# Kernel tuning notes

Hardware: AMD Instinct MI355X
Metric: run time of the kernel (lower is better)

## Reference

```python
import jax, jax.numpy as jnp
import numpy as np

TEMPERATURE = 12.5      # args_temperature
SINKHORN_EPS = 0.05     # entropic regularization replacing exact cv2.EMD
SINKHORN_ITERS = 100


def _sinkhorn_flow(cost, a, b):
    # cost: [N, hw, hw] (rows=query nodes, cols=proto nodes)
    # a: [N, hw] row marginals, b: [N, hw] col marginals (each sums to hw)
    K = jnp.exp(-cost / SINKHORN_EPS)
    v0 = jnp.ones_like(b)

    def body(v, _):
        u = a / (jnp.einsum('nuv,nv->nu', K, v) + 1e-30)
        v = b / (jnp.einsum('nuv,nu->nv', K, u) + 1e-30)
        return v, None

    v, _ = jax.lax.scan(body, v0, None, length=SINKHORN_ITERS)
    u = a / (jnp.einsum('nuv,nv->nu', K, v) + 1e-30)
    return u[:, :, None] * K * v[:, None, :]  # transport plan [N, hw, hw]


def setup_inputs() -> dict:
    key = jax.random.key(0)
    k1, k2 = jax.random.split(key)
    shape = (8, 5, 15, 640, 5, 5)  # (b, n2, n1, c, h, w)
    return {
        'in_support': jax.random.normal(k1, shape, jnp.float32),
        'in_query': jax.random.normal(k2, shape, jnp.float32),
    }


def reference(in_support, in_query):
    b, n2, n1, c, h, w = in_support.shape
    N, hw = b * n2 * n1, h * w
    S = in_support.reshape(N, c, hw)  # support/proto nodes
    Q = in_query.reshape(N, c, hw)    # query nodes

    # get_weight_vector: relu(<node, global-avg-pool(other)>) + 0.001
    w1 = jax.nn.relu(jnp.einsum('nck,nc->nk', Q, S.mean(-1))) + 0.001  # query-side
    w2 = jax.nn.relu(jnp.einsum('nck,nc->nk', S, Q.mean(-1))) + 0.001  # proto-side

    # normalize_feature: subtract per-sample channel mean ('center')
    S = S - S.mean(axis=1, keepdims=True)
    Q = Q - Q.mean(axis=1, keepdims=True)

    # cosine similarity map: sim[u, v] = cos(query_node_u, proto_node_v)
    Sn = S / jnp.maximum(jnp.linalg.norm(S, axis=1, keepdims=True), 1e-8)
    Qn = Q / jnp.maximum(jnp.linalg.norm(Q, axis=1, keepdims=True), 1e-8)
    sim = jnp.einsum('ncu,ncv->nuv', Qn, Sn)  # [N, hw, hw]

    # emd marginals: (w + 1e-5) rescaled so each sums to hw
    a = w1 + 1e-5
    a = a * (hw / a.sum(-1, keepdims=True))
    bm = w2 + 1e-5
    bm = bm * (hw / bm.sum(-1, keepdims=True))

    # OT flow on cost = 1 - sim (flow treated as a constant, like cv2 detach)
    flow = jax.lax.stop_gradient(_sinkhorn_flow(1.0 - sim, a, bm))

    return (sim * flow).sum((-1, -2)) * (TEMPERATURE / hw)  # logits [N]
```

## Files before the change

### kernel.cpp

```cpp
#include <hip/hip_runtime.h>

typedef short bf16x8 __attribute__((ext_vector_type(8)));
typedef float f32x4  __attribute__((ext_vector_type(4)));

constexpr int C  = 640;
constexpr int HW = 25;

__device__ __forceinline__ float rl(float x, int lane) {
  return __uint_as_float(__builtin_amdgcn_readlane(__float_as_uint(x), lane));
}

__device__ __forceinline__ void packpair(float x0, float x1, unsigned& h, unsigned& l) {
  unsigned u0 = __float_as_uint(x0), u1 = __float_as_uint(x1);
  h = __builtin_amdgcn_perm(u1, u0, 0x07060302u);
  float l0 = x0 - __uint_as_float(u0 & 0xFFFF0000u);
  float l1 = x1 - __uint_as_float(u1 & 0xFFFF0000u);
  l = __builtin_amdgcn_perm(__float_as_uint(l1), __float_as_uint(l0), 0x07060302u);
}

__global__ __launch_bounds__(256) void emd_fused(
    const float* __restrict__ support, const float* __restrict__ query,
    float* __restrict__ out)
{
  const int n = blockIdx.x, tid = threadIdx.x;
  const int wid = tid >> 6, lane = tid & 63;
  const int lg = lane >> 4, lr = lane & 15;

  __shared__ float accbuf[4][64][16];
  __shared__ float mombuf[4][8][64];
  __shared__ float G[625];
  __shared__ float sQv[25], sSv[25], nqv[25], nsv[25], amv[25], bmv[25], scal[2];

  const float* Qg = query   + (size_t)n * C * HW;
  const float* Sg = support + (size_t)n * C * HW;

  f32x4 acc[2][2];
  {
    f32x4 z = {0.f, 0.f, 0.f, 0.f};
    acc[0][0] = z; acc[0][1] = z; acc[1][0] = z; acc[1][1] = z;
  }
  float mq[2] = {0.f, 0.f}, mq2[2] = {0.f, 0.f};
  float ms[2] = {0.f, 0.f}, ms2[2] = {0.f, 0.f};

  #pragma unroll 1
  for (int s = 0; s < 5; ++s) {
    const int c0 = wid * 160 + s * 32 + lg * 8;
    const float* qb = Qg + c0 * HW;
    const float* sb = Sg + c0 * HW;
    bf16x8 Ah[2], Al[2], Bh[2], Bl[2];
    #pragma unroll
    for (int t = 0; t < 2; ++t) {
      const int row = t * 16 + lr;
      const bool ok = row < 25;
      float xq[8], xs[8];
      #pragma unroll
      for (int j = 0; j < 8; ++j) {
        xq[j] = ok ? qb[j * HW + row] : 0.f;
        xs[j] = ok ? sb[j * HW + row] : 0.f;
      }
      #pragma unroll
      for (int j = 0; j < 8; ++j) {
        mq[t] += xq[j]; mq2[t] = fmaf(xq[j], xq[j], mq2[t]);
        ms[t] += xs[j]; ms2[t] = fmaf(xs[j], xs[j], ms2[t]);
      }
      union { unsigned u[4]; bf16x8 v; } ah, al, bh, bl;
      #pragma unroll
      for (int jj = 0; jj < 4; ++jj) {
        packpair(xq[2 * jj], xq[2 * jj + 1], ah.u[jj], al.u[jj]);
        packpair(xs[2 * jj], xs[2 * jj + 1], bh.u[jj], bl.u[jj]);
      }
      Ah[t] = ah.v; Al[t] = al.v; Bh[t] = bh.v; Bl[t] = bl.v;
    }
    #pragma unroll
    for (int tr = 0; tr < 2; ++tr)
      #pragma unroll
      for (int tc = 0; tc < 2; ++tc) {
        acc[tr][tc] = __builtin_amdgcn_mfma_f32_16x16x32_bf16(Ah[tr], Bh[tc], acc[tr][tc], 0, 0, 0);
        acc[tr][tc] = __builtin_amdgcn_mfma_f32_16x16x32_bf16(Ah[tr], Bl[tc], acc[tr][tc], 0, 0, 0);
        acc[tr][tc] = __builtin_amdgcn_mfma_f32_16x16x32_bf16(Al[tr], Bh[tc], acc[tr][tc], 0, 0, 0);
      }
  }

  #pragma unroll
  for (int tr = 0; tr < 2; ++tr)
    #pragma unroll
    for (int tc = 0; tc < 2; ++tc)
      *reinterpret_cast<f32x4*>(&accbuf[wid][lane][(tr * 2 + tc) * 4]) = acc[tr][tc];
  mombuf[wid][0][lane] = mq[0];  mombuf[wid][1][lane] = mq[1];
  mombuf[wid][2][lane] = mq2[0]; mombuf[wid][3][lane] = mq2[1];
  mombuf[wid][4][lane] = ms[0];  mombuf[wid][5][lane] = ms[1];
  mombuf[wid][6][lane] = ms2[0]; mombuf[wid][7][lane] = ms2[1];
  __syncthreads();

  if (tid < 64) {
    #pragma unroll
    for (int q = 0; q < 4; ++q) {
      f32x4 rsum = *reinterpret_cast<const f32x4*>(&accbuf[0][lane][q * 4]);
      #pragma unroll
      for (int w = 1; w < 4; ++w)
        rsum += *reinterpret_cast<const f32x4*>(&accbuf[w][lane][q * 4]);
      const int tr = q >> 1, tc = q & 1;
      #pragma unroll
      for (int i = 0; i < 4; ++i) {
        int u = tr * 16 + (lane >> 4) * 4 + i;
        int v = tc * 16 + (lane & 15);
        if (u < 25 && v < 25) G[u * 25 + v] = rsum[i];
      }
    }
  }
  __syncthreads();

  if (tid < 25) {
    const int t = (tid < 16) ? 0 : 1, rr = tid - t * 16;
    float s = 0.f, ss = 0.f;
    #pragma unroll
    for (int w = 0; w < 4; ++w)
      #pragma unroll
      for (int gg = 0; gg < 4; ++gg) {
        s  += mombuf[w][0 + t][gg * 16 + rr];
        ss += mombuf[w][2 + t][gg * 16 + rr];
      }
    sQv[tid] = s;
    float var = ss - s * s * (1.f / C);
    nqv[tid] = fmaxf(sqrtf(fmaxf(var, 0.f)), 1e-8f);
    float rs = 0.f;
    #pragma unroll
    for (int j = 0; j < 25; ++j) rs += G[tid * 25 + j];
    amv[tid] = fmaxf(rs * (1.f / 25.f), 0.f) + 0.001f + 1e-5f;
  } else if (tid >= 32 && tid < 57) {
    const int v = tid - 32;
    const int t = (v < 16) ? 0 : 1, rr = v - t * 16;
    float s = 0.f, ss = 0.f;
    #pragma unroll
    for (int w = 0; w < 4; ++w)
      #pragma unroll
      for (int gg = 0; gg < 4; ++gg) {
        s  += mombuf[w][4 + t][gg * 16 + rr];
        ss += mombuf[w][6 + t][gg * 16 + rr];
      }
    sSv[v] = s;
    float var = ss - s * s * (1.f / C);
    nsv[v] = fmaxf(sqrtf(fmaxf(var, 0.f)), 1e-8f);
    float cs = 0.f;
    #pragma unroll
    for (int u = 0; u < 25; ++u) cs += G[u * 25 + v];
    bmv[v] = fmaxf(cs * (1.f / 25.f), 0.f) + 0.001f + 1e-5f;
  }
  __syncthreads();
  if (tid == 0)  { float s = 0.f; for (int i = 0; i < 25; ++i) s += amv[i]; scal[0] = 25.f / s; }
  if (tid == 64) { float s = 0.f; for (int i = 0; i < 25; ++i) s += bmv[i]; scal[1] = 25.f / s; }
  __syncthreads();
  for (int p = tid; p < 625; p += 256) {
    int u = p / 25, v = p % 25;
    float cov = G[p] - sQv[u] * sSv[v] * (1.f / C);
    G[p] = cov / (nqv[u] * nsv[v]);
  }
  __syncthreads();

  if (tid >= 64) return;
  const int u = (tid < 25) ? tid : 24;
  float simr[25], Krow[25], Kcol[25];
  #pragma unroll
  for (int j = 0; j < 25; ++j) simr[j] = G[u * 25 + j];
  #pragma unroll
  for (int j = 0; j < 25; ++j) Kcol[j] = __expf(-20.f * (1.f - G[j * 25 + u]));
  #pragma unroll
  for (int j = 0; j < 25; ++j) Krow[j] = __expf(-20.f * (1.f - simr[j]));
  const float a_u = amv[u] * scal[0], b_u = bmv[u] * scal[1];

  float vv = 1.0f, uu = 0.0f, vold = 1.0f;
  #pragma unroll 1
  for (int it = 0; it < 100; ++it) {
    float s0 = 0, s1 = 0, s2 = 0, s3 = 0, s4 = 0;
    #pragma unroll
    for (int j = 0; j < 25; j += 5) {
      s0 = fmaf(Krow[j + 0], rl(vv, j + 0), s0);
      s1 = fmaf(Krow[j + 1], rl(vv, j + 1), s1);
      s2 = fmaf(Krow[j + 2], rl(vv, j + 2), s2);
      s3 = fmaf(Krow[j + 3], rl(vv, j + 3), s3);
      s4 = fmaf(Krow[j + 4], rl(vv, j + 4), s4);
    }
    uu = a_u * __builtin_amdgcn_rcpf(((((s0 + s1) + (s2 + s3)) + s4) + 1e-30f));

    s0 = s1 = s2 = s3 = s4 = 0;
    #pragma unroll
    for (int j = 0; j < 25; j += 5) {
      s0 = fmaf(Kcol[j + 0], rl(uu, j + 0), s0);
      s1 = fmaf(Kcol[j + 1], rl(uu, j + 1), s1);
      s2 = fmaf(Kcol[j + 2], rl(uu, j + 2), s2);
      s3 = fmaf(Kcol[j + 3], rl(uu, j + 3), s3);
      s4 = fmaf(Kcol[j + 4], rl(uu, j + 4), s4);
    }
    vv = b_u * __builtin_amdgcn_rcpf(((((s0 + s1) + (s2 + s3)) + s4) + 1e-30f));

    if ((it & 1) == 1) {
      bool conv = fabsf(vv - vold) <= 1e-4f * fabsf(vv);
      if (__all(conv)) break;
      vold = vv;
    }
  }
  {
    float s0 = 0, s1 = 0, s2 = 0, s3 = 0, s4 = 0;
    #pragma unroll
    for (int j = 0; j < 25; j += 5) {
      s0 = fmaf(Krow[j + 0], rl(vv, j + 0), s0);
      s1 = fmaf(Krow[j + 1], rl(vv, j + 1), s1);
      s2 = fmaf(Krow[j + 2], rl(vv, j + 2), s2);
      s3 = fmaf(Krow[j + 3], rl(vv, j + 3), s3);
      s4 = fmaf(Krow[j + 4], rl(vv, j + 4), s4);
    }
    uu = a_u * __builtin_amdgcn_rcpf(((((s0 + s1) + (s2 + s3)) + s4) + 1e-30f));
  }

  float pr = 0.f;
  if (tid < 25) {
    float t0 = 0.f;
    #pragma unroll
    for (int j = 0; j < 25; ++j)
      t0 = fmaf(simr[j] * Krow[j], rl(vv, j), t0);
    pr = uu * t0;
  }
  #pragma unroll
  for (int off = 32; off; off >>= 1) pr += __shfl_xor(pr, off);
  if (tid == 0) out[n] = pr * 0.5f;
}

extern "C" void kernel_launch(void* const* d_in, const int* in_sizes, int n_in,
                              void* d_out, int out_size, void* d_ws, size_t ws_size,
                              hipStream_t stream) {
  const float* support = (const float*)d_in[0];
  const float* query   = (const float*)d_in[1];
  float* out = (float*)d_out;
  const int N = in_sizes[0] / (C * HW);
  emd_fused<<<dim3(N), dim3(256), 0, stream>>>(support, query, out);
}
```

Baseline: 24.92 us.

## Split fused kernel into channel-split Gram kernel and separate Sinkhorn kernel

The single fused kernel becomes two launches. The first computes partial Gram matrices and moment sums over half the channels per block, using 2N blocks of 320 threads, and writes them to workspace. The second kernel (64 threads per sample) adds the two halves, normalizes, and runs the Sinkhorn iterations. The aim is more parallelism and shorter per-block load chains in the memory-bound phase, and not holding 256-thread blocks while only one wave runs Sinkhorn. The cost is a second launch plus a global-memory round trip for the partials.

```diff
diff --git a/kernel.cpp b/kernel.cpp
--- a/kernel.cpp
+++ b/kernel.cpp
@@ -5,6 +5,7 @@
 
 constexpr int C  = 640;
 constexpr int HW = 25;
+constexpr int PSTRIDE = 736;
 
 __device__ __forceinline__ float rl(float x, int lane) {
   return __uint_as_float(__builtin_amdgcn_readlane(__float_as_uint(x), lane));
@@ -18,18 +19,17 @@
   l = __builtin_amdgcn_perm(__float_as_uint(l1), __float_as_uint(l0), 0x07060302u);
 }
 
-__global__ __launch_bounds__(256) void emd_fused(
+__global__ __launch_bounds__(320) void emd_gram(
     const float* __restrict__ support, const float* __restrict__ query,
-    float* __restrict__ out)
+    float* __restrict__ part)
 {
-  const int n = blockIdx.x, tid = threadIdx.x;
+  const int bid = blockIdx.x, tid = threadIdx.x;
+  const int n = bid >> 1, h = bid & 1;
   const int wid = tid >> 6, lane = tid & 63;
   const int lg = lane >> 4, lr = lane & 15;
 
-  __shared__ float accbuf[4][64][16];
-  __shared__ float mombuf[4][8][64];
-  __shared__ float G[625];
-  __shared__ float sQv[25], sSv[25], nqv[25], nsv[25], amv[25], bmv[25], scal[2];
+  __shared__ float accbuf[5][64][16];
+  __shared__ float mombuf[5][8][64];
 
   const float* Qg = query   + (size_t)n * C * HW;
   const float* Sg = support + (size_t)n * C * HW;
@@ -43,8 +43,8 @@
   float ms[2] = {0.f, 0.f}, ms2[2] = {0.f, 0.f};
 
   #pragma unroll 1
-  for (int s = 0; s < 5; ++s) {
-    const int c0 = wid * 160 + s * 32 + lg * 8;
+  for (int kc = 0; kc < 2; ++kc) {
+    const int c0 = h * 320 + wid * 64 + kc * 32 + lg * 8;
     const float* qb = Qg + c0 * HW;
     const float* sb = Sg + c0 * HW;
     bf16x8 Ah[2], Al[2], Bh[2], Bl[2];
@@ -92,34 +92,53 @@
   mombuf[wid][6][lane] = ms2[0]; mombuf[wid][7][lane] = ms2[1];
   __syncthreads();
 
+  float* w = part + (size_t)bid * PSTRIDE;
   if (tid < 64) {
     #pragma unroll
     for (int q = 0; q < 4; ++q) {
       f32x4 rsum = *reinterpret_cast<const f32x4*>(&accbuf[0][lane][q * 4]);
       #pragma unroll
-      for (int w = 1; w < 4; ++w)
-        rsum += *reinterpret_cast<const f32x4*>(&accbuf[w][lane][q * 4]);
+      for (int ww = 1; ww < 5; ++ww)
+        rsum += *reinterpret_cast<const f32x4*>(&accbuf[ww][lane][q * 4]);
       const int tr = q >> 1, tc = q & 1;
       #pragma unroll
       for (int i = 0; i < 4; ++i) {
         int u = tr * 16 + (lane >> 4) * 4 + i;
         int v = tc * 16 + (lane & 15);
-        if (u < 25 && v < 25) G[u * 25 + v] = rsum[i];
-      }
-    }
-  }
+        if (u < 25 && v < 25) w[u * 25 + v] = rsum[i];
+      }
+    }
+  } else if (tid >= 64 && tid < 164) {
+    const int mt = tid - 64;
+    const int vt = mt / 25, col = mt % 25;
+    const int base = vt * 2;
+    const int t = (col < 16) ? 0 : 1, rr = col & 15;
+    float s = 0.f;
+    #pragma unroll
+    for (int ww = 0; ww < 5; ++ww)
+      #pragma unroll
+      for (int gg = 0; gg < 4; ++gg)
+        s += mombuf[ww][base + t][gg * 16 + rr];
+    w[625 + vt * 25 + col] = s;
+  }
+}
+
+__global__ __launch_bounds__(64) void emd_sink(
+    const float* __restrict__ part, float* __restrict__ out)
+{
+  const int n = blockIdx.x, tid = threadIdx.x;
+  const float* p0 = part + (size_t)(2 * n) * PSTRIDE;
+  const float* p1 = part + (size_t)(2 * n + 1) * PSTRIDE;
+
+  __shared__ float G[625];
+  __shared__ float sQv[25], sSv[25], nqv[25], nsv[25], amv[25], bmv[25], scal[2];
+
+  for (int p = tid; p < 625; p += 64) G[p] = p0[p] + p1[p];
   __syncthreads();
 
   if (tid < 25) {
-    const int t = (tid < 16) ? 0 : 1, rr = tid - t * 16;
-    float s = 0.f, ss = 0.f;
-    #pragma unroll
-    for (int w = 0; w < 4; ++w)
-      #pragma unroll
-      for (int gg = 0; gg < 4; ++gg) {
-        s  += mombuf[w][0 + t][gg * 16 + rr];
-        ss += mombuf[w][2 + t][gg * 16 + rr];
-      }
+    float s  = p0[625 + tid] + p1[625 + tid];
+    float ss = p0[650 + tid] + p1[650 + tid];
     sQv[tid] = s;
     float var = ss - s * s * (1.f / C);
     nqv[tid] = fmaxf(sqrtf(fmaxf(var, 0.f)), 1e-8f);
@@ -129,15 +148,8 @@
     amv[tid] = fmaxf(rs * (1.f / 25.f), 0.f) + 0.001f + 1e-5f;
   } else if (tid >= 32 && tid < 57) {
     const int v = tid - 32;
-    const int t = (v < 16) ? 0 : 1, rr = v - t * 16;
-    float s = 0.f, ss = 0.f;
-    #pragma unroll
-    for (int w = 0; w < 4; ++w)
-      #pragma unroll
-      for (int gg = 0; gg < 4; ++gg) {
-        s  += mombuf[w][4 + t][gg * 16 + rr];
-        ss += mombuf[w][6 + t][gg * 16 + rr];
-      }
+    float s  = p0[675 + v] + p1[675 + v];
+    float ss = p0[700 + v] + p1[700 + v];
     sSv[v] = s;
     float var = ss - s * s * (1.f / C);
     nsv[v] = fmaxf(sqrtf(fmaxf(var, 0.f)), 1e-8f);
@@ -147,17 +159,20 @@
     bmv[v] = fmaxf(cs * (1.f / 25.f), 0.f) + 0.001f + 1e-5f;
   }
   __syncthreads();
-  if (tid == 0)  { float s = 0.f; for (int i = 0; i < 25; ++i) s += amv[i]; scal[0] = 25.f / s; }
-  if (tid == 64) { float s = 0.f; for (int i = 0; i < 25; ++i) s += bmv[i]; scal[1] = 25.f / s; }
-  __syncthreads();
-  for (int p = tid; p < 625; p += 256) {
+  if (tid == 0) {
+    float s0 = 0.f, s1 = 0.f;
+    #pragma unroll
+    for (int i = 0; i < 25; ++i) { s0 += amv[i]; s1 += bmv[i]; }
+    scal[0] = 25.f / s0; scal[1] = 25.f / s1;
+  }
+  __syncthreads();
+  for (int p = tid; p < 625; p += 64) {
     int u = p / 25, v = p % 25;
     float cov = G[p] - sQv[u] * sSv[v] * (1.f / C);
     G[p] = cov / (nqv[u] * nsv[v]);
   }
   __syncthreads();
 
-  if (tid >= 64) return;
   const int u = (tid < 25) ? tid : 24;
   float simr[25], Krow[25], Kcol[25];
   #pragma unroll
@@ -231,6 +246,8 @@
   const float* support = (const float*)d_in[0];
   const float* query   = (const float*)d_in[1];
   float* out = (float*)d_out;
+  float* partbuf = (float*)d_ws;
   const int N = in_sizes[0] / (C * HW);
-  emd_fused<<<dim3(N), dim3(256), 0, stream>>>(support, query, out);
-}
+  emd_gram<<<dim3(2 * N), dim3(320), 0, stream>>>(support, query, partbuf);
+  emd_sink<<<dim3(N),     dim3(64),  0, stream>>>(partbuf, out);
+}
```

New measurement: 31.50 us. +26.4%, slower.
